# Optimization experiments

Measured on AMD Instinct MI355X. Metric: run time of the kernel, lower is better.

## Reference

```python
import jax, jax.numpy as jnp
import numpy as np

WS = 7        # window_size
SHIFT = 3     # shift_size
NH = 12       # num_heads
HD = 32       # head_dim
C = 384       # dim
HH = 56       # height
WW = 56       # width
EPS = 1e-5


def _rel_pos_index():
    coords = np.stack(np.meshgrid(np.arange(WS), np.arange(WS), indexing='ij')).reshape(2, -1)
    rel = (coords[:, :, None] - coords[:, None, :]).transpose(1, 2, 0)
    rel[:, :, 0] += WS - 1
    rel[:, :, 1] += WS - 1
    rel[:, :, 0] *= 2 * WS - 1
    return rel.sum(-1)  # (49, 49) int


def _attn_mask():
    # shift mask, computed statically (shift_size > 0 path)
    img = np.zeros((HH, WW))
    slices = (slice(0, -WS), slice(-WS, -SHIFT), slice(-SHIFT, None))
    cnt = 0
    for hs in slices:
        for ws in slices:
            img[hs, ws] = cnt
            cnt += 1
    mw = img.reshape(HH // WS, WS, WW // WS, WS).transpose(0, 2, 1, 3).reshape(-1, WS * WS)
    diff = mw[:, None, :] - mw[:, :, None]  # (nW, 49, 49)
    return np.where(diff != 0, -100.0, 0.0).astype(np.float32)


_REL_IDX = jnp.asarray(_rel_pos_index())
_MASK = jnp.asarray(_attn_mask())


def _layernorm(x, g, b):
    mu = jnp.mean(x, axis=-1, keepdims=True)
    var = jnp.mean(jnp.square(x - mu), axis=-1, keepdims=True)
    return (x - mu) * jax.lax.rsqrt(var + EPS) * g + b


def setup_inputs() -> dict:
    key = jax.random.key(0)
    ks = jax.random.split(key, 10)
    s = 0.02
    return {
        'hidden_states': jax.random.normal(ks[0], (32, HH * WW, C), jnp.float32),
        'ln1_g': jnp.ones((C,), jnp.float32),
        'ln1_b': jnp.zeros((C,), jnp.float32),
        'qkv_w': jax.random.normal(ks[1], (3 * C, C), jnp.float32) * s,
        'qkv_b': jnp.zeros((3 * C,), jnp.float32),
        'out_w': jax.random.normal(ks[2], (C, C), jnp.float32) * s,
        'out_b': jnp.zeros((C,), jnp.float32),
        'rel_bias_table': jax.random.normal(ks[3], ((2 * WS - 1) ** 2, NH), jnp.float32) * s,
        'ln2_g': jnp.ones((C,), jnp.float32),
        'ln2_b': jnp.zeros((C,), jnp.float32),
        'fc1_w': jax.random.normal(ks[4], (4 * C, C), jnp.float32) * s,
        'fc1_b': jnp.zeros((4 * C,), jnp.float32),
        'fc2_w': jax.random.normal(ks[5], (C, 4 * C), jnp.float32) * s,
        'fc2_b': jnp.zeros((C,), jnp.float32),
        'height': HH,
        'width': WW,
    }


def reference(hidden_states, ln1_g, ln1_b, qkv_w, qkv_b, out_w, out_b,
              rel_bias_table, ln2_g, ln2_b, fc1_w, fc1_b, fc2_w, fc2_b,
              height, width):
    B = hidden_states.shape[0]
    nWh, nWw = HH // WS, WW // WS
    nW = nWh * nWw
    L = WS * WS

    shortcut = hidden_states
    x = _layernorm(hidden_states, ln1_g, ln1_b).reshape(B, HH, WW, C)
    x = jnp.roll(x, (-SHIFT, -SHIFT), axis=(1, 2))
    # window partition -> (B*nW, 49, C)
    xw = x.reshape(B, nWh, WS, nWw, WS, C).transpose(0, 1, 3, 2, 4, 5).reshape(B * nW, L, C)

    qkv = xw @ qkv_w.T + qkv_b
    q, k, v = jnp.split(qkv, 3, axis=-1)
    q = q.reshape(-1, L, NH, HD).transpose(0, 2, 1, 3)  # (N, h, 49, d)
    k = k.reshape(-1, L, NH, HD).transpose(0, 2, 1, 3)
    v = v.reshape(-1, L, NH, HD).transpose(0, 2, 1, 3)

    scale = HD ** -0.5
    attn = jnp.einsum('nhqd,nhkd->nhqk', q, k) * scale
    bias = rel_bias_table[_REL_IDX.reshape(-1)].reshape(L, L, NH).transpose(2, 0, 1)  # (h, 49, 49)
    attn = attn + bias[None]
    attn = attn.reshape(B, nW, NH, L, L) + _MASK[None, :, None]
    attn = jax.nn.softmax(attn, axis=-1).reshape(B * nW, NH, L, L)

    out = jnp.einsum('nhqk,nhkd->nhqd', attn, v).transpose(0, 2, 1, 3).reshape(B * nW, L, C)
    out = out @ out_w.T + out_b

    # window reverse + un-shift
    out = out.reshape(B, nWh, nWw, WS, WS, C).transpose(0, 1, 3, 2, 4, 5).reshape(B, HH, WW, C)
    out = jnp.roll(out, (SHIFT, SHIFT), axis=(1, 2)).reshape(B, HH * WW, C)

    x = shortcut + out  # drop_path is identity (rate 0 / eval)
    h2 = _layernorm(x, ln2_g, ln2_b)
    mlp = jax.nn.gelu(h2 @ fc1_w.T + fc1_b, approximate=False) @ fc2_w.T + fc2_b
    return x + mlp
```

## Files before the change

### kernel.cpp

```cpp
#include <hip/hip_runtime.h>
#include <cstdint>
#include <cstddef>

using u16 = unsigned short;
using u32 = unsigned int;

typedef __attribute__((ext_vector_type(8))) short bf16x8;
typedef __attribute__((ext_vector_type(4))) float f32x4;

__device__ __forceinline__ u16 f2bf(float f) {
  union { float f; u32 u; } v; v.f = f;
  u32 r = v.u + 0x7FFFu + ((v.u >> 16) & 1u);
  return (u16)(r >> 16);
}
__device__ __forceinline__ float bf2f(u16 h) {
  union { u32 u; float f; } v; v.u = ((u32)h) << 16;
  return v.f;
}

__device__ __forceinline__ void gl_lds16(const void* g, void* l) {
  __builtin_amdgcn_global_load_lds(
      (const __attribute__((address_space(1))) void*)g,
      (__attribute__((address_space(3))) void*)l, 16, 0, 0);
}

__global__ __launch_bounds__(256) void k_f2bf(const float* __restrict__ s,
                                              u16* __restrict__ d, int n) {
  int i = blockIdx.x * 256 + threadIdx.x;
  if (i < n) d[i] = f2bf(s[i]);
}

__global__ __launch_bounds__(256) void k_tbl(const float* __restrict__ relt,
                                             float* __restrict__ tbl) {
  int id = blockIdx.x * 256 + threadIdx.x;
  if (id >= 196608) return;
  int i = id & 63, j = (id >> 6) & 63;
  int wt = (id >> 12) & 3, h = id >> 14;
  float v;
  if (j >= 49) {
    v = -3e38f;
  } else {
    int ii = i < 49 ? i : 48;
    int r1 = ii / 7, c1 = ii % 7, r2 = j / 7, c2 = j % 7;
    v = relt[((r1 - r2 + 6) * 13 + (c1 - c2 + 6)) * 12 + h];
    int rr1 = (wt & 2) ? (r1 < 4 ? 1 : 2) : 0;
    int rr2 = (wt & 2) ? (r2 < 4 ? 1 : 2) : 0;
    int cc1 = (wt & 1) ? (c1 < 4 ? 1 : 2) : 0;
    int cc2 = (wt & 1) ? (c2 < 4 ? 1 : 2) : 0;
    if (rr1 != rr2 || cc1 != cc2) v -= 100.f;
  }
  tbl[id] = v;
}

template <int GATHER>
__global__ __launch_bounds__(256) void k_ln(const float* __restrict__ x,
                                            const float* __restrict__ g,
                                            const float* __restrict__ b,
                                            u16* __restrict__ out) {
  int wave = threadIdx.x >> 6, lane = threadIdx.x & 63;
  int idx = blockIdx.x * 4 + wave;
  int src;
  if (GATHER) {
    int n = idx / 49, l = idx % 49;
    int bb = n >> 6, wi = n & 63;
    int wh = wi >> 3, ww = wi & 7;
    int r = l / 7, c = l % 7;
    int sr = wh * 7 + r + 3; if (sr >= 56) sr -= 56;
    int sc = ww * 7 + c + 3; if (sc >= 56) sc -= 56;
    src = bb * 3136 + sr * 56 + sc;
  } else {
    src = idx;
  }
  const float* xi = x + (size_t)src * 384;
  float2 v[3];
  float s = 0.f, sq = 0.f;
#pragma unroll
  for (int p = 0; p < 3; ++p) {
    v[p] = *(const float2*)(xi + p * 128 + lane * 2);
    s += v[p].x + v[p].y;
    sq += v[p].x * v[p].x + v[p].y * v[p].y;
  }
#pragma unroll
  for (int o = 32; o; o >>= 1) {
    s += __shfl_xor(s, o);
    sq += __shfl_xor(sq, o);
  }
  float mu = s * (1.f / 384.f);
  float var = sq * (1.f / 384.f) - mu * mu;
  float rstd = rsqrtf(var + 1e-5f);
  u16* oo = out + (size_t)idx * 384;
#pragma unroll
  for (int p = 0; p < 3; ++p) {
    int e = p * 128 + lane * 2;
    u16 o0 = f2bf((v[p].x - mu) * rstd * g[e] + b[e]);
    u16 o1 = f2bf((v[p].y - mu) * rstd * g[e + 1] + b[e + 1]);
    u32 pk = (u32)o0 | ((u32)o1 << 16);
    *(u32*)(oo + e) = pk;
  }
}

enum { EPI_QKV = 0, EPI_PROJ = 1, EPI_GELU = 2, EPI_FC2 = 3 };

template <int EPI>
__global__ __launch_bounds__(256) void k_gemm(
    const u16* __restrict__ A, const u16* __restrict__ Bw,
    const float* __restrict__ bias, u16* __restrict__ obf,
    float* __restrict__ of32, const float* __restrict__ addsrc,
    int K, int lda, int ldb, int ldc, int NT) {
  __shared__ u16 As[128 * 64];
  __shared__ u16 Bs[128 * 64];
  const int nwg = gridDim.x;
  const int q = nwg >> 3, r = nwg & 7;
  const int xcd = blockIdx.x & 7, rank = blockIdx.x >> 3;
  const int swz = (xcd < r ? xcd * (q + 1) : r * (q + 1) + (xcd - r) * q) + rank;
  const int m0 = (swz / NT) * 128, n0 = (swz % NT) * 128;

  const int tid = threadIdx.x;
  const int w = tid >> 6, lane = tid & 63;
  const int wr = w >> 1, wc = w & 1;

  f32x4 acc[4][4] = {};

  const int lrow = lane & 15;
  const int lko = (lane >> 4) * 8;
  const int elem0 = w * 512 + lane * 8;

  for (int k0 = 0; k0 < K; k0 += 64) {
#pragma unroll
    for (int i = 0; i < 4; ++i) {
      int elem = i * 2048 + elem0;
      int row = elem >> 6, col = elem & 63;
      gl_lds16(A + (size_t)(m0 + row) * lda + k0 + col, As + i * 2048 + w * 512);
    }
#pragma unroll
    for (int i = 0; i < 4; ++i) {
      int elem = i * 2048 + elem0;
      int row = elem >> 6, col = elem & 63;
      gl_lds16(Bw + (size_t)(n0 + row) * ldb + k0 + col, Bs + i * 2048 + w * 512);
    }
    __syncthreads();
#pragma unroll
    for (int kk = 0; kk < 64; kk += 32) {
      bf16x8 af[4], bf[4];
#pragma unroll
      for (int mi = 0; mi < 4; ++mi)
        af[mi] = *(const bf16x8*)(As + (wr * 64 + mi * 16 + lrow) * 64 + kk + lko);
#pragma unroll
      for (int ni = 0; ni < 4; ++ni)
        bf[ni] = *(const bf16x8*)(Bs + (wc * 64 + ni * 16 + lrow) * 64 + kk + lko);
#pragma unroll
      for (int mi = 0; mi < 4; ++mi)
#pragma unroll
        for (int ni = 0; ni < 4; ++ni)
          acc[mi][ni] = __builtin_amdgcn_mfma_f32_16x16x32_bf16(
              af[mi], bf[ni], acc[mi][ni], 0, 0, 0);
    }
    __syncthreads();
  }

  const int erow = (lane >> 4) * 4;
  const int ecol = lane & 15;
#pragma unroll
  for (int mi = 0; mi < 4; ++mi) {
#pragma unroll
    for (int ni = 0; ni < 4; ++ni) {
      int gcol = n0 + wc * 64 + ni * 16 + ecol;
      float bv = bias[gcol];
#pragma unroll
      for (int r = 0; r < 4; ++r) {
        int grow = m0 + wr * 64 + mi * 16 + erow + r;
        float v = acc[mi][ni][r] + bv;
        if (EPI == EPI_QKV) {
          float vv = (gcol < 384) ? v * 0.17677669529663689f : v;
          obf[(size_t)grow * ldc + gcol] = f2bf(vv);
        } else if (EPI == EPI_GELU) {
          float gl = 0.5f * v * (1.f + erff(v * 0.70710678118f));
          obf[(size_t)grow * ldc + gcol] = f2bf(gl);
        } else if (EPI == EPI_PROJ) {
          int nwin = grow / 49, l = grow % 49;
          int bb = nwin >> 6, wi = nwin & 63;
          int wh = wi >> 3, ww = wi & 7;
          int rr = l / 7, cc = l % 7;
          int sr = wh * 7 + rr + 3; if (sr >= 56) sr -= 56;
          int sc = ww * 7 + cc + 3; if (sc >= 56) sc -= 56;
          size_t idx = ((size_t)(bb * 3136 + sr * 56 + sc)) * 384 + gcol;
          of32[idx] = addsrc[idx] + v;
        } else {
          size_t idx = (size_t)grow * 384 + gcol;
          of32[idx] = of32[idx] + v;
        }
      }
    }
  }
}

__global__ __launch_bounds__(64) void k_attn2(const u16* __restrict__ qkv,
                                              const float* __restrict__ tbl,
                                              u16* __restrict__ out) {
  __shared__ u16 P[64 * 64];
  const int bx = blockIdx.x;
  const int n = bx / 12, h = bx - n * 12;
  const int lane = threadIdx.x & 63;
  const int g = lane >> 4, c = lane & 15;
  const u16* base = qkv + (size_t)n * 56448 + h * 32;
  const int wi = n & 63;
  const int wt = (((wi >> 3) == 7) ? 2 : 0) | (((wi & 7) == 7) ? 1 : 0);
  const float* T = tbl + (size_t)((h << 2) | wt) * 4096;

  f32x4 st[4][4];
#pragma unroll
  for (int kj = 0; kj < 4; ++kj)
#pragma unroll
    for (int qi = 0; qi < 4; ++qi)
#pragma unroll
      for (int r = 0; r < 4; ++r)
        st[kj][qi][r] = T[(kj * 16 + g * 4 + r) * 64 + qi * 16 + c];

  bf16x8 qf[4], kf[4];
#pragma unroll
  for (int t = 0; t < 4; ++t) {
    int row = t * 16 + c; if (row > 48) row = 48;
    qf[t] = *(const bf16x8*)(base + (size_t)row * 1152 + g * 8);
    kf[t] = *(const bf16x8*)(base + (size_t)row * 1152 + 384 + g * 8);
  }

#pragma unroll
  for (int kj = 0; kj < 4; ++kj)
#pragma unroll
    for (int qi = 0; qi < 4; ++qi)
      st[kj][qi] = __builtin_amdgcn_mfma_f32_16x16x32_bf16(kf[kj], qf[qi],
                                                           st[kj][qi], 0, 0, 0);

#pragma unroll
  for (int qi = 0; qi < 4; ++qi) {
    float m = -3e38f;
#pragma unroll
    for (int kj = 0; kj < 4; ++kj)
#pragma unroll
      for (int r = 0; r < 4; ++r) m = fmaxf(m, st[kj][qi][r]);
    m = fmaxf(m, __shfl_xor(m, 16));
    m = fmaxf(m, __shfl_xor(m, 32));
    float sum = 0.f;
#pragma unroll
    for (int kj = 0; kj < 4; ++kj)
#pragma unroll
      for (int r = 0; r < 4; ++r) {
        float e = __expf(st[kj][qi][r] - m);
        st[kj][qi][r] = e;
        sum += e;
      }
    sum += __shfl_xor(sum, 16);
    sum += __shfl_xor(sum, 32);
    float inv = 1.f / sum;
    int i = qi * 16 + c;
#pragma unroll
    for (int kj = 0; kj < 4; ++kj)
#pragma unroll
      for (int hh = 0; hh < 2; ++hh) {
        u32 pk = (u32)f2bf(st[kj][qi][2 * hh] * inv) |
                 ((u32)f2bf(st[kj][qi][2 * hh + 1] * inv) << 16);
        int idx = (i * 64 + kj * 16 + g * 4 + 2 * hh) ^ ((i & 7) << 3);
        *(u32*)(P + idx) = pk;
      }
  }

  f32x4 o[4][2] = {};
#pragma unroll
  for (int k0 = 0; k0 < 2; ++k0) {
    bf16x8 pa[4], vb[2];
#pragma unroll
    for (int qi = 0; qi < 4; ++qi) {
      int qq = qi * 16 + c;
      pa[qi] = *(const bf16x8*)(P + ((qq * 64 + k0 * 32 + g * 8) ^ ((qq & 7) << 3)));
    }
#pragma unroll
    for (int ni = 0; ni < 2; ++ni) {
      union { bf16x8 v; u16 a[8]; } vu;
#pragma unroll
      for (int e = 0; e < 8; ++e) {
        int j = k0 * 32 + g * 8 + e;
        int jr = j > 48 ? 48 : j;
        vu.a[e] = base[(size_t)jr * 1152 + 768 + ni * 16 + c];
      }
      vb[ni] = vu.v;
#pragma unroll
      for (int qi = 0; qi < 4; ++qi)
        o[qi][ni] = __builtin_amdgcn_mfma_f32_16x16x32_bf16(pa[qi], vb[ni],
                                                            o[qi][ni], 0, 0, 0);
    }
  }

  u16* ob = out + (size_t)n * 18816 + h * 32;
#pragma unroll
  for (int qi = 0; qi < 4; ++qi)
#pragma unroll
    for (int r = 0; r < 4; ++r) {
      int qq = qi * 16 + g * 4 + r;
      if (qq < 49) {
#pragma unroll
        for (int ni = 0; ni < 2; ++ni)
          ob[(size_t)qq * 384 + ni * 16 + c] = f2bf(o[qi][ni][r]);
      }
    }
}

extern "C" void kernel_launch(void* const* d_in, const int* in_sizes, int n_in,
                              void* d_out, int out_size, void* d_ws,
                              size_t ws_size, hipStream_t stream) {
  const float* hidden = (const float*)d_in[0];
  const float* ln1g = (const float*)d_in[1];
  const float* ln1b = (const float*)d_in[2];
  const float* qkvw = (const float*)d_in[3];
  const float* qkvb = (const float*)d_in[4];
  const float* outw = (const float*)d_in[5];
  const float* outb = (const float*)d_in[6];
  const float* relt = (const float*)d_in[7];
  const float* ln2g = (const float*)d_in[8];
  const float* ln2b = (const float*)d_in[9];
  const float* fc1w = (const float*)d_in[10];
  const float* fc1b = (const float*)d_in[11];
  const float* fc2w = (const float*)d_in[12];
  const float* fc2b = (const float*)d_in[13];
  float* out = (float*)d_out;

  u16* wq = (u16*)d_ws;
  u16* wo = wq + 442368;
  u16* w1 = wo + 147456;
  u16* w2 = w1 + 589824;
  u16* xw = w2 + 589824;
  u16* qkv = xw + 38535168;
  u16* xn = qkv;
  u16* hbuf = xn + 38535168;
  float* tbl = (float*)wq;

  k_f2bf<<<(442368 + 255) / 256, 256, 0, stream>>>(qkvw, wq, 442368);
  k_f2bf<<<(147456 + 255) / 256, 256, 0, stream>>>(outw, wo, 147456);
  k_f2bf<<<(589824 + 255) / 256, 256, 0, stream>>>(fc1w, w1, 589824);
  k_f2bf<<<(589824 + 255) / 256, 256, 0, stream>>>(fc2w, w2, 589824);

  k_ln<1><<<25088, 256, 0, stream>>>(hidden, ln1g, ln1b, xw);

  k_gemm<EPI_QKV><<<784 * 9, 256, 0, stream>>>(
      xw, wq, qkvb, qkv, nullptr, nullptr, 384, 384, 384, 1152, 9);

  k_tbl<<<768, 256, 0, stream>>>(relt, tbl);

  k_attn2<<<24576, 64, 0, stream>>>(qkv, tbl, xw);

  k_gemm<EPI_PROJ><<<784 * 3, 256, 0, stream>>>(
      xw, wo, outb, nullptr, out, hidden, 384, 384, 384, 384, 3);

  k_ln<0><<<25088, 256, 0, stream>>>(out, ln2g, ln2b, xn);

  for (int ch = 0; ch < 2; ++ch) {
    const u16* xa = xn + (size_t)ch * 50176 * 384;
    float* oc = out + (size_t)ch * 50176 * 384;
    k_gemm<EPI_GELU><<<392 * 12, 256, 0, stream>>>(
        xa, w1, fc1b, hbuf, nullptr, nullptr, 384, 384, 384, 1536, 12);
    k_gemm<EPI_FC2><<<392 * 3, 256, 0, stream>>>(
        hbuf, w2, fc2b, nullptr, oc, nullptr, 1536, 1536, 1536, 384, 3);
  }
}
```

Baseline: 1.055 ms.

## Double-buffer GEMM LDS tiles and XOR-swizzle shared memory layout

The GEMM main loop now uses two LDS buffers per operand and prefetches the next K tile with async global-to-LDS loads while the current tile is computed. It waits with explicit vmcnt counters and raw barriers instead of __syncthreads. Staged rows are XOR-swizzled by column group to reduce LDS bank conflicts on fragment reads, and wave priority is raised around the MFMA block. This doubles LDS use to 64KB per block, which may cut occupancy.

```diff
diff --git a/kernel.cpp b/kernel.cpp
--- a/kernel.cpp
+++ b/kernel.cpp
@@ -107,8 +107,8 @@
     const float* __restrict__ bias, u16* __restrict__ obf,
     float* __restrict__ of32, const float* __restrict__ addsrc,
     int K, int lda, int ldb, int ldc, int NT) {
-  __shared__ u16 As[128 * 64];
-  __shared__ u16 Bs[128 * 64];
+  __shared__ u16 As[2][128 * 64];
+  __shared__ u16 Bs[2][128 * 64];
   const int nwg = gridDim.x;
   const int q = nwg >> 3, r = nwg & 7;
   const int xcd = blockIdx.x & 7, rank = blockIdx.x >> 3;
@@ -119,35 +119,57 @@
   const int w = tid >> 6, lane = tid & 63;
   const int wr = w >> 1, wc = w & 1;
 
+  const int srow = 8 * w + (lane >> 3);
+  const int scol = 8 * ((lane & 7) ^ (lane >> 3));
+  const int dstw = w * 512;
+  const size_t abase = (size_t)(m0 + srow) * lda + scol;
+  const size_t bbase = (size_t)(n0 + srow) * ldb + scol;
+
   f32x4 acc[4][4] = {};
-
   const int lrow = lane & 15;
-  const int lko = (lane >> 4) * 8;
-  const int elem0 = w * 512 + lane * 8;
-
-  for (int k0 = 0; k0 < K; k0 += 64) {
-#pragma unroll
-    for (int i = 0; i < 4; ++i) {
-      int elem = i * 2048 + elem0;
-      int row = elem >> 6, col = elem & 63;
-      gl_lds16(A + (size_t)(m0 + row) * lda + k0 + col, As + i * 2048 + w * 512);
-    }
-#pragma unroll
-    for (int i = 0; i < 4; ++i) {
-      int elem = i * 2048 + elem0;
-      int row = elem >> 6, col = elem & 63;
-      gl_lds16(Bw + (size_t)(n0 + row) * ldb + k0 + col, Bs + i * 2048 + w * 512);
-    }
-    __syncthreads();
+  const int g8 = (lane >> 4) * 8;
+  const int rxor = (lrow & 7) << 3;
+
+  const int NTK = K >> 6;
+#pragma unroll
+  for (int i = 0; i < 4; ++i)
+    gl_lds16(A + abase + (size_t)(32 * i) * lda, &As[0][i * 2048 + dstw]);
+#pragma unroll
+  for (int i = 0; i < 4; ++i)
+    gl_lds16(Bw + bbase + (size_t)(32 * i) * ldb, &Bs[0][i * 2048 + dstw]);
+
+  for (int t = 0; t < NTK; ++t) {
+    const int cur = t & 1;
+    if (t + 1 < NTK) {
+      const int k1 = (t + 1) << 6;
+#pragma unroll
+      for (int i = 0; i < 4; ++i)
+        gl_lds16(A + abase + (size_t)(32 * i) * lda + k1,
+                 &As[cur ^ 1][i * 2048 + dstw]);
+#pragma unroll
+      for (int i = 0; i < 4; ++i)
+        gl_lds16(Bw + bbase + (size_t)(32 * i) * ldb + k1,
+                 &Bs[cur ^ 1][i * 2048 + dstw]);
+      asm volatile("s_waitcnt vmcnt(8)" ::: "memory");
+    } else {
+      asm volatile("s_waitcnt vmcnt(0)" ::: "memory");
+    }
+    __builtin_amdgcn_s_barrier();
+    asm volatile("" ::: "memory");
+    __builtin_amdgcn_s_setprio(1);
 #pragma unroll
     for (int kk = 0; kk < 64; kk += 32) {
       bf16x8 af[4], bf[4];
 #pragma unroll
-      for (int mi = 0; mi < 4; ++mi)
-        af[mi] = *(const bf16x8*)(As + (wr * 64 + mi * 16 + lrow) * 64 + kk + lko);
-#pragma unroll
-      for (int ni = 0; ni < 4; ++ni)
-        bf[ni] = *(const bf16x8*)(Bs + (wc * 64 + ni * 16 + lrow) * 64 + kk + lko);
+      for (int mi = 0; mi < 4; ++mi) {
+        int row = wr * 64 + mi * 16 + lrow;
+        af[mi] = *(const bf16x8*)(&As[cur][row * 64 + ((kk + g8) ^ rxor)]);
+      }
+#pragma unroll
+      for (int ni = 0; ni < 4; ++ni) {
+        int row = wc * 64 + ni * 16 + lrow;
+        bf[ni] = *(const bf16x8*)(&Bs[cur][row * 64 + ((kk + g8) ^ rxor)]);
+      }
 #pragma unroll
       for (int mi = 0; mi < 4; ++mi)
 #pragma unroll
@@ -155,7 +177,10 @@
           acc[mi][ni] = __builtin_amdgcn_mfma_f32_16x16x32_bf16(
               af[mi], bf[ni], acc[mi][ni], 0, 0, 0);
     }
-    __syncthreads();
+    __builtin_amdgcn_s_setprio(0);
+    asm volatile("" ::: "memory");
+    __builtin_amdgcn_s_barrier();
+    asm volatile("" ::: "memory");
   }
 
   const int erow = (lane >> 4) * 4;
@@ -167,9 +192,9 @@
       int gcol = n0 + wc * 64 + ni * 16 + ecol;
       float bv = bias[gcol];
 #pragma unroll
-      for (int r = 0; r < 4; ++r) {
-        int grow = m0 + wr * 64 + mi * 16 + erow + r;
-        float v = acc[mi][ni][r] + bv;
+      for (int r4 = 0; r4 < 4; ++r4) {
+        int grow = m0 + wr * 64 + mi * 16 + erow + r4;
+        float v = acc[mi][ni][r4] + bv;
         if (EPI == EPI_QKV) {
           float vv = (gcol < 384) ? v * 0.17677669529663689f : v;
           obf[(size_t)grow * ldc + gcol] = f2bf(vv);
```

Measured after the change: 968.5 us. -8.2%, faster.
